# Kernel optimization log

Measured on AMD Instinct MI355X. Metric: run time of the kernel, lower is better.

The kernel has to match this reference:

```python
import jax, jax.numpy as jnp
import numpy as np

B, D, T = 8, 1024, 512
HID, NH, NL = 256, 4, 2
OUT = HID // NH  # 64 per-head dim
ALPHA = 0.2      # leaky relu slope
EPS = 1e-5       # layernorm eps


def setup_inputs() -> dict:
    key = jax.random.key(0)
    ks = jax.random.split(key, 10)
    X_obs = jax.random.normal(ks[0], (B, D, T), dtype=jnp.float32)
    mask = (jax.random.uniform(ks[1], (B, D, T)) < 0.8).astype(jnp.float32)
    W_in = jax.random.normal(ks[2], (2 * T, HID), dtype=jnp.float32) * (1.0 / np.sqrt(2 * T))
    b_in = jnp.zeros((HID,), dtype=jnp.float32)
    gat_W = jax.random.normal(ks[3], (NL, NH, HID, OUT), dtype=jnp.float32) * (1.0 / np.sqrt(HID))
    gat_a = jax.random.normal(ks[4], (NL, NH, 2 * OUT), dtype=jnp.float32) * 0.1
    ln_g = jnp.ones((NL, HID), dtype=jnp.float32)
    ln_b = jnp.zeros((NL, HID), dtype=jnp.float32)
    W_out = jax.random.normal(ks[5], (HID, T), dtype=jnp.float32) * (1.0 / np.sqrt(HID))
    b_out = jnp.zeros((T,), dtype=jnp.float32)
    return dict(X_obs=X_obs, mask=mask, W_in=W_in, b_in=b_in, gat_W=gat_W,
                gat_a=gat_a, ln_g=ln_g, ln_b=ln_b, W_out=W_out, b_out=b_out)


def _layer_norm(x, g, b):
    mu = jnp.mean(x, axis=-1, keepdims=True)
    var = jnp.mean((x - mu) ** 2, axis=-1, keepdims=True)
    return (x - mu) * jax.lax.rsqrt(var + EPS) * g + b


def _gat_forward(X_obs, mask, W_in, b_in, gat_W, gat_a, ln_g, ln_b, W_out, b_out):
    # mean-impute per (d, t) position across batch
    obs_sum = jnp.sum(X_obs * mask, axis=0, keepdims=True)
    obs_cnt = jnp.sum(mask, axis=0, keepdims=True)
    pos_mean = obs_sum / (obs_cnt + 1e-10)
    X_mean = X_obs * mask + (1.0 - mask) * pos_mean

    x = jnp.concatenate([X_mean, mask], axis=-1)       # (B, D, 2T)
    h = x @ W_in + b_in                                 # (B, N, HID)

    for l in range(NL):
        Wl = gat_W[l]                                   # (H, HID, OUT)
        a_left = gat_a[l, :, :OUT]                      # (H, OUT)
        a_right = gat_a[l, :, OUT:]                     # (H, OUT)
        hW = jnp.einsum('bnd,hde->bhne', h, Wl)         # (B, H, N, OUT)
        # e_ij = leakyrelu(a_left . h_i + a_right . h_j) -- avoids O(N^2 * 2d) concat
        s_l = jnp.einsum('bhne,he->bhn', hW, a_left)
        s_r = jnp.einsum('bhne,he->bhn', hW, a_right)
        e = jax.nn.leaky_relu(s_l[..., :, None] + s_r[..., None, :], ALPHA)  # (B,H,N,N)
        attn = jax.nn.softmax(e, axis=-1)
        head_out = jnp.einsum('bhnm,bhme->bhne', attn, hW)                   # (B,H,N,OUT)
        h_new = jnp.transpose(head_out, (0, 2, 1, 3)).reshape(h.shape[0], h.shape[1], HID)
        h = _layer_norm(h + h_new, ln_g[l], ln_b[l])

    return h @ W_out + b_out                            # (B, D, T)


def reference(X_obs, mask, W_in, b_in, gat_W, gat_a, ln_g, ln_b, W_out, b_out):
    return _gat_forward(X_obs, mask, W_in, b_in, gat_W, gat_a, ln_g, ln_b, W_out, b_out)
```

## Files before the change

kernel.cpp:

```cpp
#include <hip/hip_runtime.h>
#include <hip/hip_bf16.h>

constexpr int B_   = 8;
constexpr int D_   = 1024;
constexpr int T_   = 512;
constexpr int HID_ = 256;
constexpr int NH_  = 4;
constexpr int NL_  = 2;
constexpr float ALPHA_ = 0.2f;
constexpr float EPS_   = 1e-5f;
constexpr int OUT_ = 64;
constexpr int M_ = B_ * D_;
constexpr int DT_ = D_ * T_;
constexpr int KIN_ = 2 * T_;

typedef __attribute__((ext_vector_type(8))) short short8;
typedef __attribute__((ext_vector_type(4))) float floatx4;

__device__ __forceinline__ unsigned short f2bf(float f) {
    unsigned int u = __float_as_uint(f);
    unsigned int r = u + 0x7fffu + ((u >> 16) & 1u);
    return (unsigned short)(r >> 16);
}
__device__ __forceinline__ unsigned int kenc(float f) {
    unsigned int u = __float_as_uint(f);
    return (u & 0x80000000u) ? ~u : (u | 0x80000000u);
}
__device__ __forceinline__ float kdec(unsigned int k) {
    unsigned int u = (k & 0x80000000u) ? (k ^ 0x80000000u) : ~k;
    return __uint_as_float(u);
}

__global__ __launch_bounds__(256) void prep_k(const float* __restrict__ X,
                                              const float* __restrict__ Mk,
                                              const float* __restrict__ W_in,
                                              const float* __restrict__ gatW,
                                              const float* __restrict__ W_out,
                                              unsigned short* __restrict__ Ain,
                                              unsigned short* __restrict__ Wt_in,
                                              unsigned short* __restrict__ Wcat,
                                              unsigned short* __restrict__ WtO,
                                              unsigned int* __restrict__ rmaxkey) {
    int bx = blockIdx.x;
    if (bx < 512) {
        int idx4 = (bx * 256 + threadIdx.x) * 4;
        int t = idx4 & (T_ - 1);
        int d = idx4 >> 9;
        float4 x[B_], m[B_];
        float4 s = {0, 0, 0, 0}, c = {0, 0, 0, 0};
#pragma unroll
        for (int b = 0; b < B_; b++) {
            x[b] = *(const float4*)&X[(size_t)b * DT_ + idx4];
            m[b] = *(const float4*)&Mk[(size_t)b * DT_ + idx4];
            s.x += x[b].x * m[b].x; s.y += x[b].y * m[b].y;
            s.z += x[b].z * m[b].z; s.w += x[b].w * m[b].w;
            c.x += m[b].x; c.y += m[b].y; c.z += m[b].z; c.w += m[b].w;
        }
        float4 pm;
        pm.x = s.x / (c.x + 1e-10f); pm.y = s.y / (c.y + 1e-10f);
        pm.z = s.z / (c.z + 1e-10f); pm.w = s.w / (c.w + 1e-10f);
#pragma unroll
        for (int b = 0; b < B_; b++) {
            size_t row = (size_t)b * D_ + d;
            ushort4 xm, mk;
            xm.x = f2bf(x[b].x * m[b].x + (1.f - m[b].x) * pm.x);
            xm.y = f2bf(x[b].y * m[b].y + (1.f - m[b].y) * pm.y);
            xm.z = f2bf(x[b].z * m[b].z + (1.f - m[b].z) * pm.z);
            xm.w = f2bf(x[b].w * m[b].w + (1.f - m[b].w) * pm.w);
            mk.x = f2bf(m[b].x); mk.y = f2bf(m[b].y);
            mk.z = f2bf(m[b].z); mk.w = f2bf(m[b].w);
            *(ushort4*)&Ain[row * KIN_ + t]      = xm;
            *(ushort4*)&Ain[row * KIN_ + T_ + t] = mk;
        }
    } else {
        int idx = (bx - 512) * 256 + threadIdx.x;
        if (idx < 64) rmaxkey[idx] = 0u;
        if (idx < 262144) {
            int n = idx >> 10, k = idx & 1023;
            Wt_in[idx] = f2bf(W_in[(size_t)k * HID_ + n]);
        } else if (idx < 393216) {
            int j = idx - 262144;
            int l = j >> 16, n = (j >> 8) & 255, k = j & 255;
            int h = n >> 6, e = n & 63;
            Wcat[j] = f2bf(gatW[(((size_t)(l * NH_ + h) * HID_) + k) * OUT_ + e]);
        } else {
            int j = idx - 393216;
            int n = j >> 8, k = j & 255;
            WtO[j] = f2bf(W_out[(size_t)k * T_ + n]);
        }
    }
}

template <int MODE>
__global__ __launch_bounds__(256) void gemm_bf16_k(
        const unsigned short* __restrict__ A,
        const unsigned short* __restrict__ Bt,
        const float* __restrict__ bias,
        float* __restrict__ C,
        unsigned short* __restrict__ Cb,
        const float* __restrict__ ga,
        float* __restrict__ s_l,
        float* __restrict__ s_r,
        unsigned int* __restrict__ rmaxkey,
        int Nsz, int Ksz) {
    __shared__ __align__(16) unsigned short As[2][64 * 72];
    __shared__ __align__(16) unsigned short Bs[2][64 * 72];
    int tid = threadIdx.x;
    int wave = tid >> 6, lane = tid & 63;
    int q = lane >> 4, r16 = lane & 15;
    int rowbase = blockIdx.y * 64;
    int colbase = blockIdx.x * 64;

    int srow = tid >> 3, sk = (tid & 7) * 8;
    const unsigned short* Ap0 = A + (size_t)(rowbase + srow) * Ksz + sk;
    const unsigned short* Ap1 = A + (size_t)(rowbase + srow + 32) * Ksz + sk;
    const unsigned short* Bp0 = Bt + (size_t)(colbase + srow) * Ksz + sk;
    const unsigned short* Bp1 = Bt + (size_t)(colbase + srow + 32) * Ksz + sk;
    int la0 = srow * 72 + sk, la1 = (srow + 32) * 72 + sk;

    floatx4 acc[4];
#pragma unroll
    for (int i = 0; i < 4; i++) acc[i] = (floatx4)0.f;

    uint4 pa0 = *(const uint4*)Ap0, pa1 = *(const uint4*)Ap1;
    uint4 pb0 = *(const uint4*)Bp0, pb1 = *(const uint4*)Bp1;
    *(uint4*)&As[0][la0] = pa0;
    *(uint4*)&As[0][la1] = pa1;
    *(uint4*)&Bs[0][la0] = pb0;
    *(uint4*)&Bs[0][la1] = pb1;

    int nk = Ksz >> 6;
    for (int it = 0; it < nk; it++) {
        int cur = it & 1;
        __syncthreads();
        if (it + 1 < nk) {
            int kt = (it + 1) << 6;
            pa0 = *(const uint4*)(Ap0 + kt);
            pa1 = *(const uint4*)(Ap1 + kt);
            pb0 = *(const uint4*)(Bp0 + kt);
            pb1 = *(const uint4*)(Bp1 + kt);
        }
#pragma unroll
        for (int t = 0; t < 2; t++) {
            short8 a = *(const short8*)&As[cur][(wave * 16 + r16) * 72 + t * 32 + q * 8];
#pragma unroll
            for (int ni = 0; ni < 4; ni++) {
                short8 b = *(const short8*)&Bs[cur][(ni * 16 + r16) * 72 + t * 32 + q * 8];
                acc[ni] = __builtin_amdgcn_mfma_f32_16x16x32_bf16(a, b, acc[ni], 0, 0, 0);
            }
        }
        if (it + 1 < nk) {
            int nxt = cur ^ 1;
            *(uint4*)&As[nxt][la0] = pa0;
            *(uint4*)&As[nxt][la1] = pa1;
            *(uint4*)&Bs[nxt][la0] = pb0;
            *(uint4*)&Bs[nxt][la1] = pb1;
        }
    }
    if constexpr (MODE == 2) {
        int bhh = ((rowbase >> 10) << 2) + blockIdx.x;
        int nb = (rowbase & (D_ - 1)) + wave * 16;
#pragma unroll
        for (int ni = 0; ni < 4; ni++) {
            int e = ni * 16 + r16;
            ushort4 pk;
            pk.x = f2bf(acc[ni][0]);
            pk.y = f2bf(acc[ni][1]);
            pk.z = f2bf(acc[ni][2]);
            pk.w = f2bf(acc[ni][3]);
            *(ushort4*)&Cb[((size_t)(bhh * 64 + e) << 10) + nb + q * 4] = pk;
        }
        const float* gab = ga + blockIdx.x * 2 * OUT_;
        float al4[4], ar4[4];
#pragma unroll
        for (int ni = 0; ni < 4; ni++) {
            al4[ni] = gab[ni * 16 + r16];
            ar4[ni] = gab[OUT_ + ni * 16 + r16];
        }
        float slv[4], srv[4];
#pragma unroll
        for (int rr = 0; rr < 4; rr++) {
            float s1 = 0.f, s2 = 0.f;
#pragma unroll
            for (int ni = 0; ni < 4; ni++) {
                s1 += acc[ni][rr] * al4[ni];
                s2 += acc[ni][rr] * ar4[ni];
            }
            slv[rr] = s1;
            srv[rr] = s2;
        }
#pragma unroll
        for (int off = 1; off < 16; off <<= 1) {
#pragma unroll
            for (int rr = 0; rr < 4; rr++) {
                slv[rr] += __shfl_xor(slv[rr], off, 64);
                srv[rr] += __shfl_xor(srv[rr], off, 64);
            }
        }
        {
            int rsel = r16 & 3;
            float sv = (rsel == 0) ? slv[0] : (rsel == 1) ? slv[1] : (rsel == 2) ? slv[2] : slv[3];
            float rv = (rsel == 0) ? srv[0] : (rsel == 1) ? srv[1] : (rsel == 2) ? srv[2] : srv[3];
            int n = nb + q * 4 + rsel;
            if (r16 < 4)                 s_l[bhh * D_ + n] = sv;
            else if (r16 >= 8 && r16 < 12) s_r[bhh * D_ + n] = rv;
        }
        float mx = fmaxf(fmaxf(srv[0], srv[1]), fmaxf(srv[2], srv[3]));
        mx = fmaxf(mx, __shfl_xor(mx, 16, 64));
        mx = fmaxf(mx, __shfl_xor(mx, 32, 64));
        if (lane == 0) atomicMax(&rmaxkey[bhh], kenc(mx));
    } else {
#pragma unroll
        for (int rr = 0; rr < 4; rr++) {
            int row = rowbase + wave * 16 + q * 4 + rr;
#pragma unroll
            for (int ni = 0; ni < 4; ni++) {
                int col = colbase + ni * 16 + r16;
                float v = acc[ni][rr] + (bias ? bias[col] : 0.f);
                C[(size_t)row * Nsz + col] = v;
                if constexpr (MODE == 1) Cb[(size_t)row * Nsz + col] = f2bf(v);
            }
        }
    }
}

__global__ __launch_bounds__(256) void attn_k(const unsigned short* __restrict__ hwT,
                                              const float* __restrict__ sl_g,
                                              const float* __restrict__ sr_g,
                                              const unsigned int* __restrict__ rmaxkey,
                                              float* __restrict__ pacc,
                                              float* __restrict__ pden) {
    int bh = blockIdx.x;
    int b = bh >> 2, h = bh & 3;
    int half = blockIdx.z;
    int mb = half * 512;
    int tid = threadIdx.x;
    int wave = tid >> 6, lane = tid & 63;
    int q = lane >> 4, r16 = lane & 15;

    __shared__ float srs[512];
    __shared__ __align__(16) unsigned short Vt[2][64][136];

    *(float2*)&srs[tid * 2] = *(const float2*)&sr_g[bh * D_ + mb + tid * 2];

    float rm = kdec(rmaxkey[bh]);
    int row0 = blockIdx.y * 64 + wave * 16;
    float sl = sl_g[bh * D_ + row0 + r16];
    float xm = sl + rm;
    float Mn = fmaxf(xm, ALPHA_ * xm);

    floatx4 acc[4];
#pragma unroll
    for (int i = 0; i < 4; i++) acc[i] = (floatx4)0.f;
    float dsum = 0.f;

    const unsigned short* vbase = hwT + ((size_t)(bh * 64) << 10) + mb;
    int se[4], sp[4];
#pragma unroll
    for (int i = 0; i < 4; i++) {
        int s = tid + i * 256;
        se[i] = s >> 4;
        sp[i] = (s & 15) * 8;
    }

    uint4 pre[4];
#pragma unroll
    for (int i = 0; i < 4; i++)
        pre[i] = *(const uint4*)&vbase[((size_t)se[i] << 10) + sp[i]];
#pragma unroll
    for (int i = 0; i < 4; i++)
        *(uint4*)&Vt[0][se[i]][sp[i]] = pre[i];
    __syncthreads();

    for (int c = 0; c < 4; c++) {
        int cur = c & 1;
        if (c < 3) {
            int mo = (c + 1) * 128;
#pragma unroll
            for (int i = 0; i < 4; i++)
                pre[i] = *(const uint4*)&vbase[((size_t)se[i] << 10) + mo + sp[i]];
        }
#pragma unroll
        for (int kk = 0; kk < 128; kk += 32) {
            int m0 = c * 128 + kk + q * 8;
            float4 s0 = *(const float4*)&srs[m0];
            float4 s1 = *(const float4*)&srs[m0 + 4];
            float sr8[8] = {s0.x, s0.y, s0.z, s0.w, s1.x, s1.y, s1.z, s1.w};
            float p[8];
#pragma unroll
            for (int j = 0; j < 8; j++) {
                float x = sl + sr8[j];
                float e = fmaxf(x, ALPHA_ * x);
                float pj = __expf(e - Mn);
                dsum += pj;
                p[j] = pj;
            }
            union { unsigned int u[4]; short8 s8; } cv;
#pragma unroll
            for (int j = 0; j < 4; j++) {
                unsigned int lo = (__float_as_uint(p[2 * j]) + 0x8000u) >> 16;
                unsigned int hi = (__float_as_uint(p[2 * j + 1]) + 0x8000u) & 0xffff0000u;
                cv.u[j] = hi | lo;
            }
#pragma unroll
            for (int ni = 0; ni < 4; ni++) {
                short8 bfr = *(const short8*)&Vt[cur][ni * 16 + r16][kk + q * 8];
                acc[ni] = __builtin_amdgcn_mfma_f32_16x16x32_bf16(cv.s8, bfr, acc[ni], 0, 0, 0);
            }
        }
        if (c < 3) {
#pragma unroll
            for (int i = 0; i < 4; i++)
                *(uint4*)&Vt[cur ^ 1][se[i]][sp[i]] = pre[i];
        }
        __syncthreads();
    }
    dsum += __shfl_xor(dsum, 16);
    dsum += __shfl_xor(dsum, 32);
    size_t gr0 = (size_t)b * D_ + row0;
    if (lane < 16) pden[((size_t)half * M_ + gr0 + r16) * NH_ + h] = dsum;
#pragma unroll
    for (int rr = 0; rr < 4; rr++) {
        int rloc = q * 4 + rr;
        size_t grow = gr0 + rloc;
#pragma unroll
        for (int ni = 0; ni < 4; ni++) {
            pacc[((size_t)half * M_ + grow) * HID_ + h * OUT_ + ni * 16 + r16] = acc[ni][rr];
        }
    }
}

__global__ __launch_bounds__(256) void addln_k(float* __restrict__ h,
                                               const float* __restrict__ pacc,
                                               const float* __restrict__ pden,
                                               const float* __restrict__ g,
                                               const float* __restrict__ bb,
                                               unsigned short* __restrict__ hbf) {
    int wave = threadIdx.x >> 6, lane = threadIdx.x & 63;
    size_t row = (size_t)blockIdx.x * 4 + wave;
    float4 a  = *(const float4*)&h[row * HID_ + lane * 4];
    float4 p0 = *(const float4*)&pacc[row * HID_ + lane * 4];
    float4 p1 = *(const float4*)&pacc[((size_t)M_ + row) * HID_ + lane * 4];
    int hh = lane >> 4;
    float den = pden[row * NH_ + hh] + pden[((size_t)M_ + row) * NH_ + hh];
    float inv = 1.f / den;
    float4 v = {a.x + (p0.x + p1.x) * inv, a.y + (p0.y + p1.y) * inv,
                a.z + (p0.z + p1.z) * inv, a.w + (p0.w + p1.w) * inv};
    float s = v.x + v.y + v.z + v.w;
#pragma unroll
    for (int off = 1; off < 64; off <<= 1) s += __shfl_xor(s, off, 64);
    float mu = s * (1.f / HID_);
    float4 d = {v.x - mu, v.y - mu, v.z - mu, v.w - mu};
    float s2 = d.x * d.x + d.y * d.y + d.z * d.z + d.w * d.w;
#pragma unroll
    for (int off = 1; off < 64; off <<= 1) s2 += __shfl_xor(s2, off, 64);
    float rs = rsqrtf(s2 * (1.f / HID_) + EPS_);
    float4 gg = *(const float4*)&g[lane * 4];
    float4 bbv = *(const float4*)&bb[lane * 4];
    float4 res;
    res.x = d.x * rs * gg.x + bbv.x;
    res.y = d.y * rs * gg.y + bbv.y;
    res.z = d.z * rs * gg.z + bbv.z;
    res.w = d.w * rs * gg.w + bbv.w;
    *(float4*)&h[row * HID_ + lane * 4] = res;
    ushort4 pk = {f2bf(res.x), f2bf(res.y), f2bf(res.z), f2bf(res.w)};
    *(ushort4*)&hbf[row * HID_ + lane * 4] = pk;
}

extern "C" void kernel_launch(void* const* d_in, const int* in_sizes, int n_in,
                              void* d_out, int out_size, void* d_ws, size_t ws_size,
                              hipStream_t stream) {
    const float* X_obs = (const float*)d_in[0];
    const float* mask  = (const float*)d_in[1];
    const float* W_in  = (const float*)d_in[2];
    const float* b_in  = (const float*)d_in[3];
    const float* gat_W = (const float*)d_in[4];
    const float* gat_a = (const float*)d_in[5];
    const float* ln_g  = (const float*)d_in[6];
    const float* ln_b  = (const float*)d_in[7];
    const float* W_out = (const float*)d_in[8];
    const float* b_out = (const float*)d_in[9];
    float* out = (float*)d_out;

    char* base = (char*)d_ws;
    unsigned short* Ain  = (unsigned short*)base;
    unsigned short* hwT  = (unsigned short*)base;
    float* pacc = (float*)(base + (4u << 20));
    float* pden = (float*)(base + (20u << 20));
    float* hbuf = (float*)(base + (21u << 20));
    unsigned short* hbf   = (unsigned short*)(base + (29u << 20));
    unsigned short* Wt_in = (unsigned short*)(base + (33u << 20));
    unsigned short* Wcat  = Wt_in + (size_t)HID_ * KIN_;
    unsigned short* WtO   = Wcat + (size_t)NL_ * HID_ * HID_;
    float* slb = (float*)(WtO + (size_t)T_ * HID_);
    float* srb = slb + B_ * NH_ * D_;
    unsigned int* rmaxkey = (unsigned int*)(srb + B_ * NH_ * D_);

    prep_k<<<2560, 256, 0, stream>>>(X_obs, mask, W_in, gat_W, W_out,
                                     Ain, Wt_in, Wcat, WtO, rmaxkey);

    gemm_bf16_k<1><<<dim3(HID_ / 64, M_ / 64), 256, 0, stream>>>(
        Ain, Wt_in, b_in, hbuf, hbf, nullptr, nullptr, nullptr, nullptr,
        HID_, KIN_);

    for (int l = 0; l < NL_; l++) {
        gemm_bf16_k<2><<<dim3(HID_ / 64, M_ / 64), 256, 0, stream>>>(
            hbf, Wcat + (size_t)l * HID_ * HID_, nullptr, nullptr, hwT,
            gat_a + (size_t)l * NH_ * 2 * OUT_, slb, srb, rmaxkey + l * 32,
            HID_, HID_);
        attn_k<<<dim3(B_ * NH_, D_ / 64, 2), 256, 0, stream>>>(
            hwT, slb, srb, rmaxkey + l * 32, pacc, pden);
        addln_k<<<M_ / 4, 256, 0, stream>>>(hbuf, pacc, pden,
                                            ln_g + (size_t)l * HID_,
                                            ln_b + (size_t)l * HID_, hbf);
    }

    gemm_bf16_k<0><<<dim3(T_ / 64, M_ / 64), 256, 0, stream>>>(
        hbf, WtO, b_out, out, nullptr, nullptr, nullptr, nullptr, nullptr,
        T_, HID_);
}
```

Before: 216.5 us.

## Fuse residual-add LayerNorm into attention via last-block atomic counter

Merges the separate add+LayerNorm kernel into the attention kernel. Each block writes its partial results, bumps a per-(batch, row-tile) atomic counter, and the eighth arriving block (4 heads x 2 key halves) does the residual add and LayerNorm for those 64 rows. This removes one kernel launch per layer and the gap between kernels. It also pre-scales the scores by log2(e) so exp2f replaces __expf. The cost is threadfence overhead and an LN tail done by only a few blocks, which may serialize the end of the kernel.

```diff
diff --git a/kernel.cpp b/kernel.cpp
--- a/kernel.cpp
+++ b/kernel.cpp
@@ -9,6 +9,7 @@
 constexpr int NL_  = 2;
 constexpr float ALPHA_ = 0.2f;
 constexpr float EPS_   = 1e-5f;
+constexpr float LOG2E_ = 1.4426950408889634f;
 constexpr int OUT_ = 64;
 constexpr int M_ = B_ * D_;
 constexpr int DT_ = D_ * T_;
@@ -40,7 +41,8 @@
                                               unsigned short* __restrict__ Wt_in,
                                               unsigned short* __restrict__ Wcat,
                                               unsigned short* __restrict__ WtO,
-                                              unsigned int* __restrict__ rmaxkey) {
+                                              unsigned int* __restrict__ rmaxkey,
+                                              int* __restrict__ cnt) {
     int bx = blockIdx.x;
     if (bx < 512) {
         int idx4 = (bx * 256 + threadIdx.x) * 4;
@@ -74,6 +76,7 @@
         }
     } else {
         int idx = (bx - 512) * 256 + threadIdx.x;
+        if (idx < 256) cnt[idx] = 0;
         if (idx < 64) rmaxkey[idx] = 0u;
         if (idx < 262144) {
             int n = idx >> 10, k = idx & 1023;
@@ -224,14 +227,19 @@
     }
 }
 
-__global__ __launch_bounds__(256) void attn_k(const unsigned short* __restrict__ hwT,
-                                              const float* __restrict__ sl_g,
-                                              const float* __restrict__ sr_g,
-                                              const unsigned int* __restrict__ rmaxkey,
-                                              float* __restrict__ pacc,
-                                              float* __restrict__ pden) {
+__global__ __launch_bounds__(256) void attnln_k(const unsigned short* __restrict__ hwT,
+                                                const float* __restrict__ sl_g,
+                                                const float* __restrict__ sr_g,
+                                                const unsigned int* __restrict__ rmaxkey,
+                                                float* __restrict__ pacc,
+                                                float* __restrict__ pden,
+                                                float* __restrict__ h,
+                                                const float* __restrict__ g,
+                                                const float* __restrict__ bb,
+                                                unsigned short* __restrict__ hbf,
+                                                int* __restrict__ cnt) {
     int bh = blockIdx.x;
-    int b = bh >> 2, h = bh & 3;
+    int b = bh >> 2, hd = bh & 3;
     int half = blockIdx.z;
     int mb = half * 512;
     int tid = threadIdx.x;
@@ -240,12 +248,17 @@
 
     __shared__ float srs[512];
     __shared__ __align__(16) unsigned short Vt[2][64][136];
-
-    *(float2*)&srs[tid * 2] = *(const float2*)&sr_g[bh * D_ + mb + tid * 2];
-
-    float rm = kdec(rmaxkey[bh]);
+    __shared__ int ord_s;
+
+    {
+        float2 sv = *(const float2*)&sr_g[bh * D_ + mb + tid * 2];
+        sv.x *= LOG2E_; sv.y *= LOG2E_;
+        *(float2*)&srs[tid * 2] = sv;
+    }
+
+    float rm = kdec(rmaxkey[bh]) * LOG2E_;
     int row0 = blockIdx.y * 64 + wave * 16;
-    float sl = sl_g[bh * D_ + row0 + r16];
+    float sl = sl_g[bh * D_ + row0 + r16] * LOG2E_;
     float xm = sl + rm;
     float Mn = fmaxf(xm, ALPHA_ * xm);
 
@@ -291,7 +304,7 @@
             for (int j = 0; j < 8; j++) {
                 float x = sl + sr8[j];
                 float e = fmaxf(x, ALPHA_ * x);
-                float pj = __expf(e - Mn);
+                float pj = exp2f(e - Mn);
                 dsum += pj;
                 p[j] = pj;
             }
@@ -318,53 +331,54 @@
     dsum += __shfl_xor(dsum, 16);
     dsum += __shfl_xor(dsum, 32);
     size_t gr0 = (size_t)b * D_ + row0;
-    if (lane < 16) pden[((size_t)half * M_ + gr0 + r16) * NH_ + h] = dsum;
+    if (lane < 16) pden[((size_t)half * M_ + gr0 + r16) * NH_ + hd] = dsum;
 #pragma unroll
     for (int rr = 0; rr < 4; rr++) {
-        int rloc = q * 4 + rr;
-        size_t grow = gr0 + rloc;
+        size_t grow = gr0 + q * 4 + rr;
 #pragma unroll
         for (int ni = 0; ni < 4; ni++) {
-            pacc[((size_t)half * M_ + grow) * HID_ + h * OUT_ + ni * 16 + r16] = acc[ni][rr];
-        }
-    }
-}
-
-__global__ __launch_bounds__(256) void addln_k(float* __restrict__ h,
-                                               const float* __restrict__ pacc,
-                                               const float* __restrict__ pden,
-                                               const float* __restrict__ g,
-                                               const float* __restrict__ bb,
-                                               unsigned short* __restrict__ hbf) {
-    int wave = threadIdx.x >> 6, lane = threadIdx.x & 63;
-    size_t row = (size_t)blockIdx.x * 4 + wave;
-    float4 a  = *(const float4*)&h[row * HID_ + lane * 4];
-    float4 p0 = *(const float4*)&pacc[row * HID_ + lane * 4];
-    float4 p1 = *(const float4*)&pacc[((size_t)M_ + row) * HID_ + lane * 4];
+            pacc[((size_t)half * M_ + grow) * HID_ + hd * OUT_ + ni * 16 + r16] = acc[ni][rr];
+        }
+    }
+
+    __threadfence();
+    if (tid == 0) ord_s = atomicAdd(&cnt[b * 16 + blockIdx.y], 1);
+    __syncthreads();
+    if (ord_s != 7) return;
+    __threadfence();
+
+    size_t rbase = (size_t)b * D_ + blockIdx.y * 64 + wave * 16;
     int hh = lane >> 4;
-    float den = pden[row * NH_ + hh] + pden[((size_t)M_ + row) * NH_ + hh];
-    float inv = 1.f / den;
-    float4 v = {a.x + (p0.x + p1.x) * inv, a.y + (p0.y + p1.y) * inv,
-                a.z + (p0.z + p1.z) * inv, a.w + (p0.w + p1.w) * inv};
-    float s = v.x + v.y + v.z + v.w;
-#pragma unroll
-    for (int off = 1; off < 64; off <<= 1) s += __shfl_xor(s, off, 64);
-    float mu = s * (1.f / HID_);
-    float4 d = {v.x - mu, v.y - mu, v.z - mu, v.w - mu};
-    float s2 = d.x * d.x + d.y * d.y + d.z * d.z + d.w * d.w;
-#pragma unroll
-    for (int off = 1; off < 64; off <<= 1) s2 += __shfl_xor(s2, off, 64);
-    float rs = rsqrtf(s2 * (1.f / HID_) + EPS_);
-    float4 gg = *(const float4*)&g[lane * 4];
-    float4 bbv = *(const float4*)&bb[lane * 4];
-    float4 res;
-    res.x = d.x * rs * gg.x + bbv.x;
-    res.y = d.y * rs * gg.y + bbv.y;
-    res.z = d.z * rs * gg.z + bbv.z;
-    res.w = d.w * rs * gg.w + bbv.w;
-    *(float4*)&h[row * HID_ + lane * 4] = res;
-    ushort4 pk = {f2bf(res.x), f2bf(res.y), f2bf(res.z), f2bf(res.w)};
-    *(ushort4*)&hbf[row * HID_ + lane * 4] = pk;
+#pragma unroll 4
+    for (int r = 0; r < 16; r++) {
+        size_t row = rbase + r;
+        float4 a  = *(const float4*)&h[row * HID_ + lane * 4];
+        float4 p0 = *(const float4*)&pacc[row * HID_ + lane * 4];
+        float4 p1 = *(const float4*)&pacc[((size_t)M_ + row) * HID_ + lane * 4];
+        float den = pden[row * NH_ + hh] + pden[((size_t)M_ + row) * NH_ + hh];
+        float inv = 1.f / den;
+        float4 v = {a.x + (p0.x + p1.x) * inv, a.y + (p0.y + p1.y) * inv,
+                    a.z + (p0.z + p1.z) * inv, a.w + (p0.w + p1.w) * inv};
+        float s = v.x + v.y + v.z + v.w;
+#pragma unroll
+        for (int off = 1; off < 64; off <<= 1) s += __shfl_xor(s, off, 64);
+        float mu = s * (1.f / HID_);
+        float4 d = {v.x - mu, v.y - mu, v.z - mu, v.w - mu};
+        float s2 = d.x * d.x + d.y * d.y + d.z * d.z + d.w * d.w;
+#pragma unroll
+        for (int off = 1; off < 64; off <<= 1) s2 += __shfl_xor(s2, off, 64);
+        float rs = rsqrtf(s2 * (1.f / HID_) + EPS_);
+        float4 gg = *(const float4*)&g[lane * 4];
+        float4 bbv = *(const float4*)&bb[lane * 4];
+        float4 res;
+        res.x = d.x * rs * gg.x + bbv.x;
+        res.y = d.y * rs * gg.y + bbv.y;
+        res.z = d.z * rs * gg.z + bbv.z;
+        res.w = d.w * rs * gg.w + bbv.w;
+        *(float4*)&h[row * HID_ + lane * 4] = res;
+        ushort4 pk = {f2bf(res.x), f2bf(res.y), f2bf(res.z), f2bf(res.w)};
+        *(ushort4*)&hbf[row * HID_ + lane * 4] = pk;
+    }
 }
 
 extern "C" void kernel_launch(void* const* d_in, const int* in_sizes, int n_in,
@@ -395,9 +409,10 @@
     float* slb = (float*)(WtO + (size_t)T_ * HID_);
     float* srb = slb + B_ * NH_ * D_;
     unsigned int* rmaxkey = (unsigned int*)(srb + B_ * NH_ * D_);
+    int* cnt = (int*)(rmaxkey + 64);
 
     prep_k<<<2560, 256, 0, stream>>>(X_obs, mask, W_in, gat_W, W_out,
-                                     Ain, Wt_in, Wcat, WtO, rmaxkey);
+                                     Ain, Wt_in, Wcat, WtO, rmaxkey, cnt);
 
     gemm_bf16_k<1><<<dim3(HID_ / 64, M_ / 64), 256, 0, stream>>>(
         Ain, Wt_in, b_in, hbuf, hbf, nullptr, nullptr, nullptr, nullptr,
@@ -408,11 +423,10 @@
             hbf, Wcat + (size_t)l * HID_ * HID_, nullptr, nullptr, hwT,
             gat_a + (size_t)l * NH_ * 2 * OUT_, slb, srb, rmaxkey + l * 32,
             HID_, HID_);
-        attn_k<<<dim3(B_ * NH_, D_ / 64, 2), 256, 0, stream>>>(
-            hwT, slb, srb, rmaxkey + l * 32, pacc, pden);
-        addln_k<<<M_ / 4, 256, 0, stream>>>(hbuf, pacc, pden,
-                                            ln_g + (size_t)l * HID_,
-                                            ln_b + (size_t)l * HID_, hbf);
+        attnln_k<<<dim3(B_ * NH_, D_ / 64, 2), 256, 0, stream>>>(
+            hwT, slb, srb, rmaxkey + l * 32, pacc, pden,
+            hbuf, ln_g + (size_t)l * HID_, ln_b + (size_t)l * HID_, hbf,
+            cnt + l * 128);
     }
 
     gemm_bf16_k<0><<<dim3(T_ / 64, M_ / 64), 256, 0, stream>>>(
```

After: 557.8 us. +157.6%, slower.

## Drop split-K attention partials, normalize in-kernel, and keep residual only in bf16

Applied to the files above, without the earlier changes.

The attention kernel no longer splits the key range into two halves. Each block now loops over all 1024 keys, divides by the softmax denominator itself, and writes one normalized fp32 head output. This removes the pacc/pden partial buffers and the matching reads in add+layernorm. The fp32 residual copy is also dropped: the residual is read back from the bf16 hidden state, and exp is rewritten as exp2 with prescaled logits. In exchange the attention grid has half as many blocks, which lowers parallelism, and the residual path loses precision.

```diff
diff --git a/kernel.cpp b/kernel.cpp
--- a/kernel.cpp
+++ b/kernel.cpp
@@ -9,6 +9,7 @@
 constexpr int NL_  = 2;
 constexpr float ALPHA_ = 0.2f;
 constexpr float EPS_   = 1e-5f;
+constexpr float LOG2E_ = 1.4426950408889634f;
 constexpr int OUT_ = 64;
 constexpr int M_ = B_ * D_;
 constexpr int DT_ = D_ * T_;
@@ -21,6 +22,9 @@
     unsigned int u = __float_as_uint(f);
     unsigned int r = u + 0x7fffu + ((u >> 16) & 1u);
     return (unsigned short)(r >> 16);
+}
+__device__ __forceinline__ float bf2f(unsigned short u) {
+    return __uint_as_float((unsigned int)u << 16);
 }
 __device__ __forceinline__ unsigned int kenc(float f) {
     unsigned int u = __float_as_uint(f);
@@ -217,8 +221,8 @@
             for (int ni = 0; ni < 4; ni++) {
                 int col = colbase + ni * 16 + r16;
                 float v = acc[ni][rr] + (bias ? bias[col] : 0.f);
-                C[(size_t)row * Nsz + col] = v;
-                if constexpr (MODE == 1) Cb[(size_t)row * Nsz + col] = f2bf(v);
+                if constexpr (MODE == 0) C[(size_t)row * Nsz + col] = v;
+                else                     Cb[(size_t)row * Nsz + col] = f2bf(v);
             }
         }
     }
@@ -228,24 +232,26 @@
                                               const float* __restrict__ sl_g,
                                               const float* __restrict__ sr_g,
                                               const unsigned int* __restrict__ rmaxkey,
-                                              float* __restrict__ pacc,
-                                              float* __restrict__ pden) {
+                                              float* __restrict__ hnew) {
     int bh = blockIdx.x;
     int b = bh >> 2, h = bh & 3;
-    int half = blockIdx.z;
-    int mb = half * 512;
     int tid = threadIdx.x;
     int wave = tid >> 6, lane = tid & 63;
     int q = lane >> 4, r16 = lane & 15;
 
-    __shared__ float srs[512];
+    __shared__ float srs[D_];
     __shared__ __align__(16) unsigned short Vt[2][64][136];
-
-    *(float2*)&srs[tid * 2] = *(const float2*)&sr_g[bh * D_ + mb + tid * 2];
-
-    float rm = kdec(rmaxkey[bh]);
+    __shared__ float den_lds[64];
+
+    {
+        float4 sv = *(const float4*)&sr_g[bh * D_ + tid * 4];
+        sv.x *= LOG2E_; sv.y *= LOG2E_; sv.z *= LOG2E_; sv.w *= LOG2E_;
+        *(float4*)&srs[tid * 4] = sv;
+    }
+
+    float rm = kdec(rmaxkey[bh]) * LOG2E_;
     int row0 = blockIdx.y * 64 + wave * 16;
-    float sl = sl_g[bh * D_ + row0 + r16];
+    float sl = sl_g[bh * D_ + row0 + r16] * LOG2E_;
     float xm = sl + rm;
     float Mn = fmaxf(xm, ALPHA_ * xm);
 
@@ -254,7 +260,7 @@
     for (int i = 0; i < 4; i++) acc[i] = (floatx4)0.f;
     float dsum = 0.f;
 
-    const unsigned short* vbase = hwT + ((size_t)(bh * 64) << 10) + mb;
+    const unsigned short* vbase = hwT + ((size_t)(bh * 64) << 10);
     int se[4], sp[4];
 #pragma unroll
     for (int i = 0; i < 4; i++) {
@@ -272,9 +278,9 @@
         *(uint4*)&Vt[0][se[i]][sp[i]] = pre[i];
     __syncthreads();
 
-    for (int c = 0; c < 4; c++) {
+    for (int c = 0; c < 8; c++) {
         int cur = c & 1;
-        if (c < 3) {
+        if (c < 7) {
             int mo = (c + 1) * 128;
 #pragma unroll
             for (int i = 0; i < 4; i++)
@@ -291,7 +297,7 @@
             for (int j = 0; j < 8; j++) {
                 float x = sl + sr8[j];
                 float e = fmaxf(x, ALPHA_ * x);
-                float pj = __expf(e - Mn);
+                float pj = exp2f(e - Mn);
                 dsum += pj;
                 p[j] = pj;
             }
@@ -308,7 +314,7 @@
                 acc[ni] = __builtin_amdgcn_mfma_f32_16x16x32_bf16(cv.s8, bfr, acc[ni], 0, 0, 0);
             }
         }
-        if (c < 3) {
+        if (c < 7) {
 #pragma unroll
             for (int i = 0; i < 4; i++)
                 *(uint4*)&Vt[cur ^ 1][se[i]][sp[i]] = pre[i];
@@ -317,35 +323,30 @@
     }
     dsum += __shfl_xor(dsum, 16);
     dsum += __shfl_xor(dsum, 32);
-    size_t gr0 = (size_t)b * D_ + row0;
-    if (lane < 16) pden[((size_t)half * M_ + gr0 + r16) * NH_ + h] = dsum;
+    if (q == 0) den_lds[wave * 16 + r16] = dsum;
+    __syncthreads();
 #pragma unroll
     for (int rr = 0; rr < 4; rr++) {
         int rloc = q * 4 + rr;
-        size_t grow = gr0 + rloc;
+        float rden = 1.f / den_lds[wave * 16 + rloc];
+        size_t grow = (size_t)(b * D_ + blockIdx.y * 64 + wave * 16 + rloc);
 #pragma unroll
         for (int ni = 0; ni < 4; ni++) {
-            pacc[((size_t)half * M_ + grow) * HID_ + h * OUT_ + ni * 16 + r16] = acc[ni][rr];
-        }
-    }
-}
-
-__global__ __launch_bounds__(256) void addln_k(float* __restrict__ h,
-                                               const float* __restrict__ pacc,
-                                               const float* __restrict__ pden,
+            hnew[grow * HID_ + h * OUT_ + ni * 16 + r16] = acc[ni][rr] * rden;
+        }
+    }
+}
+
+__global__ __launch_bounds__(256) void addln_k(unsigned short* __restrict__ hbf,
+                                               const float* __restrict__ hn,
                                                const float* __restrict__ g,
-                                               const float* __restrict__ bb,
-                                               unsigned short* __restrict__ hbf) {
+                                               const float* __restrict__ bb) {
     int wave = threadIdx.x >> 6, lane = threadIdx.x & 63;
     size_t row = (size_t)blockIdx.x * 4 + wave;
-    float4 a  = *(const float4*)&h[row * HID_ + lane * 4];
-    float4 p0 = *(const float4*)&pacc[row * HID_ + lane * 4];
-    float4 p1 = *(const float4*)&pacc[((size_t)M_ + row) * HID_ + lane * 4];
-    int hh = lane >> 4;
-    float den = pden[row * NH_ + hh] + pden[((size_t)M_ + row) * NH_ + hh];
-    float inv = 1.f / den;
-    float4 v = {a.x + (p0.x + p1.x) * inv, a.y + (p0.y + p1.y) * inv,
-                a.z + (p0.z + p1.z) * inv, a.w + (p0.w + p1.w) * inv};
+    ushort4 hb = *(const ushort4*)&hbf[row * HID_ + lane * 4];
+    float4 r = *(const float4*)&hn[row * HID_ + lane * 4];
+    float4 v = {bf2f(hb.x) + r.x, bf2f(hb.y) + r.y,
+                bf2f(hb.z) + r.z, bf2f(hb.w) + r.w};
     float s = v.x + v.y + v.z + v.w;
 #pragma unroll
     for (int off = 1; off < 64; off <<= 1) s += __shfl_xor(s, off, 64);
@@ -357,13 +358,11 @@
     float rs = rsqrtf(s2 * (1.f / HID_) + EPS_);
     float4 gg = *(const float4*)&g[lane * 4];
     float4 bbv = *(const float4*)&bb[lane * 4];
-    float4 res;
-    res.x = d.x * rs * gg.x + bbv.x;
-    res.y = d.y * rs * gg.y + bbv.y;
-    res.z = d.z * rs * gg.z + bbv.z;
-    res.w = d.w * rs * gg.w + bbv.w;
-    *(float4*)&h[row * HID_ + lane * 4] = res;
-    ushort4 pk = {f2bf(res.x), f2bf(res.y), f2bf(res.z), f2bf(res.w)};
+    ushort4 pk;
+    pk.x = f2bf(d.x * rs * gg.x + bbv.x);
+    pk.y = f2bf(d.y * rs * gg.y + bbv.y);
+    pk.z = f2bf(d.z * rs * gg.z + bbv.z);
+    pk.w = f2bf(d.w * rs * gg.w + bbv.w);
     *(ushort4*)&hbf[row * HID_ + lane * 4] = pk;
 }
 
@@ -385,11 +384,9 @@
     char* base = (char*)d_ws;
     unsigned short* Ain  = (unsigned short*)base;
     unsigned short* hwT  = (unsigned short*)base;
-    float* pacc = (float*)(base + (4u << 20));
-    float* pden = (float*)(base + (20u << 20));
-    float* hbuf = (float*)(base + (21u << 20));
-    unsigned short* hbf   = (unsigned short*)(base + (29u << 20));
-    unsigned short* Wt_in = (unsigned short*)(base + (33u << 20));
+    float* hnew = (float*)(base + (4u << 20));
+    unsigned short* hbf   = (unsigned short*)(base + (16u << 20));
+    unsigned short* Wt_in = (unsigned short*)(base + (24u << 20));
     unsigned short* Wcat  = Wt_in + (size_t)HID_ * KIN_;
     unsigned short* WtO   = Wcat + (size_t)NL_ * HID_ * HID_;
     float* slb = (float*)(WtO + (size_t)T_ * HID_);
@@ -400,7 +397,7 @@
                                      Ain, Wt_in, Wcat, WtO, rmaxkey);
 
     gemm_bf16_k<1><<<dim3(HID_ / 64, M_ / 64), 256, 0, stream>>>(
-        Ain, Wt_in, b_in, hbuf, hbf, nullptr, nullptr, nullptr, nullptr,
+        Ain, Wt_in, b_in, nullptr, hbf, nullptr, nullptr, nullptr, nullptr,
         HID_, KIN_);
 
     for (int l = 0; l < NL_; l++) {
@@ -408,11 +405,11 @@
             hbf, Wcat + (size_t)l * HID_ * HID_, nullptr, nullptr, hwT,
             gat_a + (size_t)l * NH_ * 2 * OUT_, slb, srb, rmaxkey + l * 32,
             HID_, HID_);
-        attn_k<<<dim3(B_ * NH_, D_ / 64, 2), 256, 0, stream>>>(
-            hwT, slb, srb, rmaxkey + l * 32, pacc, pden);
-        addln_k<<<M_ / 4, 256, 0, stream>>>(hbuf, pacc, pden,
+        attn_k<<<dim3(B_ * NH_, D_ / 64), 256, 0, stream>>>(
+            hwT, slb, srb, rmaxkey + l * 32, hnew);
+        addln_k<<<M_ / 4, 256, 0, stream>>>(hbf, hnew,
                                             ln_g + (size_t)l * HID_,
-                                            ln_b + (size_t)l * HID_, hbf);
+                                            ln_b + (size_t)l * HID_);
     }
 
     gemm_bf16_k<0><<<dim3(T_ / 64, M_ / 64), 256, 0, stream>>>(
```

New measurement: 231.4 us. +6.9%, slower.
